# Optimization experiments

Measured on AMD Instinct MI355X. Metric: run time of the kernel, lower is better.

Reference implementation:

```python
import jax, jax.numpy as jnp
import numpy as np

B, T, HID = 2, 4096, 1024
NH, DK, DV = 8, 128, 128
CONV_K = 4
CHUNK = 64


def short_conv_silu(x, w):
    # causal depthwise conv1d, x: [B,T,D], w: [D,K]
    K = w.shape[1]
    xp = jnp.pad(x, ((0, 0), (K - 1, 0), (0, 0)))
    out = sum(xp[:, i:i + x.shape[1], :] * w[:, i] for i in range(K))
    return jax.nn.silu(out)


def hadamard_fm(x, w1, b1, w2, b2):
    # per-head feature map: Linear(x)*Linear(x), x: [B,T,H,D]
    return (jnp.einsum('bthd,ed->bthe', x, w1) + b1) * (jnp.einsum('bthd,ed->bthe', x, w2) + b2)


def chunk_linear_attn(q, k, v, scale):
    # causal linear attention via chunked scan. q,k,v: [B,T,H,D]
    Bq, Tq, H, Dk = q.shape
    Dv = v.shape[-1]
    nc = Tq // CHUNK
    q = (q * scale).reshape(Bq, nc, CHUNK, H, Dk).transpose(1, 0, 2, 3, 4)
    k = k.reshape(Bq, nc, CHUNK, H, Dk).transpose(1, 0, 2, 3, 4)
    v = v.reshape(Bq, nc, CHUNK, H, Dv).transpose(1, 0, 2, 3, 4)
    mask = jnp.tril(jnp.ones((CHUNK, CHUNK), dtype=bool))

    def step(S, inp):
        qc, kc, vc = inp  # [B,C,H,D]
        attn = jnp.einsum('bihk,bjhk->bhij', qc, kc)
        attn = jnp.where(mask, attn, 0.0)
        o = jnp.einsum('bhij,bjhv->bihv', attn, vc) + jnp.einsum('bihk,bhkv->bihv', qc, S)
        S = S + jnp.einsum('bihk,bihv->bhkv', kc, vc)
        return S, o

    S0 = jnp.zeros((Bq, H, Dk, Dv), q.dtype)
    _, o = jax.lax.scan(step, S0, (q, k, v))  # o: [nc,B,C,H,Dv]
    return o.transpose(1, 0, 2, 3, 4).reshape(Bq, Tq, H, Dv)


def setup_inputs() -> dict:
    key = jax.random.key(0)
    ks = jax.random.split(key, 16)
    s = 0.02
    inp = {
        'hidden_states': jax.random.normal(ks[0], (B, T, HID), jnp.float32),
        'wq': jax.random.normal(ks[1], (HID, HID), jnp.float32) * s,
        'wk': jax.random.normal(ks[2], (HID, HID), jnp.float32) * s,
        'wv': jax.random.normal(ks[3], (HID, HID), jnp.float32) * s,
        'wo': jax.random.normal(ks[4], (HID, HID), jnp.float32) * s,
        'conv_q': jax.random.normal(ks[5], (HID, CONV_K), jnp.float32) * 0.2,
        'conv_k': jax.random.normal(ks[6], (HID, CONV_K), jnp.float32) * 0.2,
        'conv_v': jax.random.normal(ks[7], (HID, CONV_K), jnp.float32) * 0.2,
        'fmq_w1': jax.random.normal(ks[8], (DK, DK), jnp.float32) * s,
        'fmq_b1': jnp.zeros((DK,), jnp.float32),
        'fmq_w2': jax.random.normal(ks[9], (DK, DK), jnp.float32) * s,
        'fmq_b2': jnp.zeros((DK,), jnp.float32),
        'fmk_w1': jax.random.normal(ks[10], (DK, DK), jnp.float32) * s,
        'fmk_b1': jnp.zeros((DK,), jnp.float32),
        'fmk_w2': jax.random.normal(ks[11], (DK, DK), jnp.float32) * s,
        'fmk_b2': jnp.zeros((DK,), jnp.float32),
    }
    return inp


def reference(hidden_states, wq, wk, wv, wo, conv_q, conv_k, conv_v,
              fmq_w1, fmq_b1, fmq_w2, fmq_b2, fmk_w1, fmk_b1, fmk_w2, fmk_b2):
    q = short_conv_silu(hidden_states @ wq.T, conv_q)
    k = short_conv_silu(hidden_states @ wk.T, conv_k)
    v = short_conv_silu(hidden_states @ wv.T, conv_v)
    q = q.reshape(B, T, NH, DK)
    k = k.reshape(B, T, NH, DK)
    v = v.reshape(B, T, NH, DV)
    q = hadamard_fm(q, fmq_w1, fmq_b1, fmq_w2, fmq_b2)
    k = hadamard_fm(k, fmk_w1, fmk_b1, fmk_w2, fmk_b2)
    scale = DK ** -0.5
    o = chunk_linear_attn(q, k, v, scale)
    return o.reshape(B, T, NH * DV) @ wo.T
```

## Files before the change

kernel.cpp:

```cpp
#include <hip/hip_runtime.h>
#include <cstdint>
#include <cstddef>

#define T_SEQ 4096
#define BATCH 2
#define HIDDEN 1024
#define NHEAD 8
#define DKV 128
#define BT (BATCH * T_SEQ)
#define NCH 64
#define CHUNK_L 64
#define QSCALE 0.08838834764831845f
#define SCALE_P 1024.0f
#define SCALE_O 8192.0f
#define OEPS 0.7071067811865476f

typedef _Float16 half8 __attribute__((ext_vector_type(8)));
typedef float floatx4 __attribute__((ext_vector_type(4)));

union HBits { _Float16 h; unsigned short u; };

__global__ void cast_f32_f16(const float* __restrict__ X, _Float16* __restrict__ Y, int n8)
{
    int idx = blockIdx.x * 256 + threadIdx.x;
    if (idx < n8) {
        float4 a = ((const float4*)X)[idx * 2];
        float4 b = ((const float4*)X)[idx * 2 + 1];
        half8 h = { (_Float16)a.x, (_Float16)a.y, (_Float16)a.z, (_Float16)a.w,
                    (_Float16)b.x, (_Float16)b.y, (_Float16)b.z, (_Float16)b.w };
        *(half8*)&Y[idx * 8] = h;
    }
}

__global__ void cast8_f32_f16(const float* __restrict__ s0, const float* __restrict__ s1,
                              const float* __restrict__ s2, const float* __restrict__ s3,
                              const float* __restrict__ s4, const float* __restrict__ s5,
                              const float* __restrict__ s6, const float* __restrict__ s7,
                              _Float16* __restrict__ d0, _Float16* __restrict__ d1,
                              _Float16* __restrict__ d2, _Float16* __restrict__ d3,
                              _Float16* __restrict__ d4, _Float16* __restrict__ d5,
                              _Float16* __restrict__ d6, _Float16* __restrict__ d7,
                              int nbig, int nsmall)
{
    int sel = blockIdx.y;
    const float* src; _Float16* dst; int n8;
    switch (sel) {
        case 0: src = s0; dst = d0; n8 = nbig; break;
        case 1: src = s1; dst = d1; n8 = nbig; break;
        case 2: src = s2; dst = d2; n8 = nbig; break;
        case 3: src = s3; dst = d3; n8 = nbig; break;
        case 4: src = s4; dst = d4; n8 = nsmall; break;
        case 5: src = s5; dst = d5; n8 = nsmall; break;
        case 6: src = s6; dst = d6; n8 = nsmall; break;
        default: src = s7; dst = d7; n8 = nsmall; break;
    }
    int idx = blockIdx.x * 256 + threadIdx.x;
    if (idx < n8) {
        float4 u = ((const float4*)src)[idx * 2];
        float4 v = ((const float4*)src)[idx * 2 + 1];
        half8 h = { (_Float16)u.x, (_Float16)u.y, (_Float16)u.z, (_Float16)u.w,
                    (_Float16)v.x, (_Float16)v.y, (_Float16)v.z, (_Float16)v.w };
        *(half8*)&dst[idx * 8] = h;
    }
}

__global__ __launch_bounds__(256) void gemm_nt_f16_h16(const _Float16* __restrict__ A,
                                                       const _Float16* __restrict__ W,
                                                       _Float16* __restrict__ C,
                                                       int M, int N, int K)
{
    __shared__ _Float16 As[128 * 64];
    __shared__ _Float16 Ws[128 * 64];
    const int nwg = gridDim.x * gridDim.y;
    const int bid = blockIdx.y * gridDim.x + blockIdx.x;
    const int swz = (bid & 7) * (nwg >> 3) + (bid >> 3);
    const int bm = (swz / gridDim.x) * 128;
    const int bn = (swz % gridDim.x) * 128;
    const int tid = threadIdx.x;
    const int w = tid >> 6;
    const int l = tid & 63;
    const int wm = (w >> 1) * 64;
    const int wn = (w & 1) * 64;
    const int lane16 = l & 15;
    const int quad = l >> 4;
    const int srow = w * 8 + (l >> 3);
    const int skh = ((l & 7) ^ (l >> 3)) * 8;
    const int rsw = lane16 & 7;

    floatx4 acc[4][4];
#pragma unroll
    for (int i = 0; i < 4; ++i)
#pragma unroll
        for (int j = 0; j < 4; ++j)
            acc[i][j] = (floatx4){0.f, 0.f, 0.f, 0.f};

    for (int k0 = 0; k0 < K; k0 += 64) {
#pragma unroll
        for (int c = 0; c < 4; ++c) {
            int row = c * 32 + srow;
            const _Float16* ga = A + (size_t)(bm + row) * K + k0 + skh;
            const _Float16* gw = W + (size_t)(bn + row) * K + k0 + skh;
            __builtin_amdgcn_global_load_lds(
                (const __attribute__((address_space(1))) void*)ga,
                (__attribute__((address_space(3))) void*)(As + c * 2048 + w * 512), 16, 0, 0);
            __builtin_amdgcn_global_load_lds(
                (const __attribute__((address_space(1))) void*)gw,
                (__attribute__((address_space(3))) void*)(Ws + c * 2048 + w * 512), 16, 0, 0);
        }
        __syncthreads();

#pragma unroll
        for (int s = 0; s < 2; ++s) {
            const int pc = (((s * 4 + quad) ^ rsw)) * 8;
            half8 a[4], b[4];
#pragma unroll
            for (int i = 0; i < 4; ++i) {
                a[i] = *(const half8*)&As[(wm + i * 16 + lane16) * 64 + pc];
                b[i] = *(const half8*)&Ws[(wn + i * 16 + lane16) * 64 + pc];
            }
#pragma unroll
            for (int i = 0; i < 4; ++i)
#pragma unroll
                for (int j = 0; j < 4; ++j)
                    acc[i][j] = __builtin_amdgcn_mfma_f32_16x16x32_f16(a[i], b[j], acc[i][j], 0, 0, 0);
        }
        __syncthreads();
    }
#pragma unroll
    for (int i = 0; i < 4; ++i)
#pragma unroll
        for (int j = 0; j < 4; ++j)
#pragma unroll
            for (int r = 0; r < 4; ++r)
                C[(size_t)(bm + wm + i * 16 + quad * 4 + r) * N + bn + wn + j * 16 + lane16] =
                    (_Float16)acc[i][j][r];
}

__global__ __launch_bounds__(256) void gemm_nt_f16_f32(const _Float16* __restrict__ A,
                                                       const _Float16* __restrict__ W,
                                                       float* __restrict__ C,
                                                       int M, int N, int K, float scale)
{
    __shared__ _Float16 As[128 * 64];
    __shared__ _Float16 Ws[128 * 64];
    const int nwg = gridDim.x * gridDim.y;
    const int bid = blockIdx.y * gridDim.x + blockIdx.x;
    const int swz = (bid & 7) * (nwg >> 3) + (bid >> 3);
    const int bm = (swz / gridDim.x) * 128;
    const int bn = (swz % gridDim.x) * 128;
    const int tid = threadIdx.x;
    const int w = tid >> 6;
    const int l = tid & 63;
    const int wm = (w >> 1) * 64;
    const int wn = (w & 1) * 64;
    const int lane16 = l & 15;
    const int quad = l >> 4;
    const int srow = w * 8 + (l >> 3);
    const int skh = ((l & 7) ^ (l >> 3)) * 8;
    const int rsw = lane16 & 7;

    floatx4 acc[4][4];
#pragma unroll
    for (int i = 0; i < 4; ++i)
#pragma unroll
        for (int j = 0; j < 4; ++j)
            acc[i][j] = (floatx4){0.f, 0.f, 0.f, 0.f};

    for (int k0 = 0; k0 < K; k0 += 64) {
#pragma unroll
        for (int c = 0; c < 4; ++c) {
            int row = c * 32 + srow;
            const _Float16* ga = A + (size_t)(bm + row) * K + k0 + skh;
            const _Float16* gw = W + (size_t)(bn + row) * K + k0 + skh;
            __builtin_amdgcn_global_load_lds(
                (const __attribute__((address_space(1))) void*)ga,
                (__attribute__((address_space(3))) void*)(As + c * 2048 + w * 512), 16, 0, 0);
            __builtin_amdgcn_global_load_lds(
                (const __attribute__((address_space(1))) void*)gw,
                (__attribute__((address_space(3))) void*)(Ws + c * 2048 + w * 512), 16, 0, 0);
        }
        __syncthreads();

#pragma unroll
        for (int s = 0; s < 2; ++s) {
            const int pc = (((s * 4 + quad) ^ rsw)) * 8;
            half8 a[4], b[4];
#pragma unroll
            for (int i = 0; i < 4; ++i) {
                a[i] = *(const half8*)&As[(wm + i * 16 + lane16) * 64 + pc];
                b[i] = *(const half8*)&Ws[(wn + i * 16 + lane16) * 64 + pc];
            }
#pragma unroll
            for (int i = 0; i < 4; ++i)
#pragma unroll
                for (int j = 0; j < 4; ++j)
                    acc[i][j] = __builtin_amdgcn_mfma_f32_16x16x32_f16(a[i], b[j], acc[i][j], 0, 0, 0);
        }
        __syncthreads();
    }
#pragma unroll
    for (int i = 0; i < 4; ++i)
#pragma unroll
        for (int j = 0; j < 4; ++j)
#pragma unroll
            for (int r = 0; r < 4; ++r)
                C[(size_t)(bm + wm + i * 16 + quad * 4 + r) * N + bn + wn + j * 16 + lane16] =
                    acc[i][j][r] * scale;
}

__global__ __launch_bounds__(256) void conv_silu_T(const _Float16* __restrict__ X, int ldx,
                                                   const float* __restrict__ Wc,
                                                   _Float16* __restrict__ VT)
{
    __shared__ _Float16 xs[67 * 64];
    const int bx = blockIdx.x;
    const int t0 = (bx & 63) * 64;
    const int dt = ((bx >> 6) & 15) * 64;
    const int z = bx >> 10;
    const int tid = threadIdx.x;

#pragma unroll
    for (int i = 0; i < 3; ++i) {
        int p = tid + 256 * i;
        if (p < 536) {
            int row = p >> 3, d8 = (p & 7) * 8;
            int t = t0 - 3 + row;
            half8 v;
            if (t >= 0)
                v = *(const half8*)&X[((size_t)z * T_SEQ + t) * ldx + dt + d8];
            else
                v = (half8){0, 0, 0, 0, 0, 0, 0, 0};
            *(half8*)&xs[row * 64 + d8] = v;
        }
    }
    __syncthreads();

    const int d = tid & 63;
    const int dg = dt + d;
    float4 w = *(const float4*)&Wc[dg * 4];
#pragma unroll
    for (int u = 0; u < 2; ++u) {
        int tg = (tid >> 6) + u * 4;
        half8 o;
#pragma unroll
        for (int s = 0; s < 8; ++s) {
            int base = (tg * 8 + s + 3) * 64 + d;
            float acc = (float)xs[base] * w.w
                      + (float)xs[base - 64] * w.z
                      + (float)xs[base - 128] * w.y
                      + (float)xs[base - 192] * w.x;
            o[s] = (_Float16)(acc / (1.f + __expf(-acc)));
        }
        *(half8*)&VT[((size_t)z * HIDDEN + dg) * T_SEQ + t0 + tg * 8] = o;
    }
}

#define XIN_LD 136
__global__ __launch_bounds__(256) void convfm(const _Float16* __restrict__ QKV, int ldx,
                                              const float* __restrict__ Wcq,
                                              const float* __restrict__ Wck,
                                              const _Float16* __restrict__ Wfm,
                                              const float* __restrict__ Bq1,
                                              const float* __restrict__ Bq2,
                                              const float* __restrict__ Bk1,
                                              const float* __restrict__ Bk2,
                                              _Float16* __restrict__ OUTq,
                                              _Float16* __restrict__ OUTk)
{
    const int sel = blockIdx.z;
    const float* Wc = sel ? Wck : Wcq;
    const _Float16* W1h = Wfm + (sel ? 2 * 16384 : 0);
    const _Float16* W2h = Wfm + (sel ? 3 * 16384 : 16384);
    const float* B1 = sel ? Bk1 : Bq1;
    const float* B2 = sel ? Bk2 : Bq2;
    _Float16* OUT = sel ? OUTk : OUTq;

    __shared__ _Float16 xin[67 * XIN_LD];
    __shared__ _Float16 xs[4 * 64 * 32];
    const int t0 = blockIdx.x * 64;
    const int h = blockIdx.y;
    const int tid = threadIdx.x;
    const int w = tid >> 6;
    const int l = tid & 63;
    const int lane16 = l & 15;
    const int quad = l >> 4;
    const bool batch_start = (t0 & (T_SEQ - 1)) == 0;
    const int ebase = w * 32 + lane16;

    half8 pb1[2], pb2[2];
    float b1v[2], b2v[2];
#pragma unroll
    for (int nt = 0; nt < 2; ++nt) {
        pb1[nt] = *(const half8*)&W1h[(size_t)(ebase + nt * 16) * DKV + quad * 8];
        pb2[nt] = *(const half8*)&W2h[(size_t)(ebase + nt * 16) * DKV + quad * 8];
        b1v[nt] = B1[ebase + nt * 16];
        b2v[nt] = B2[ebase + nt * 16];
    }

    for (int p = tid; p < 67 * 16; p += 256) {
        int row = p >> 4, cg = p & 15;
        half8 v;
        if (batch_start && row < 3)
            v = (half8){0, 0, 0, 0, 0, 0, 0, 0};
        else
            v = *(const half8*)&QKV[(size_t)(t0 - 3 + row) * ldx + sel * HIDDEN + h * DKV + cg * 8];
        *(half8*)&xin[row * XIN_LD + cg * 8] = v;
    }
    __syncthreads();

    {
        const int doct = tid & 15;
        const int d0 = doct * 8;
        const int rq = (tid >> 4) * 4;
        const int u = doct >> 2;
        const int col = d0 & 31;

        float w0[8], w1[8], w2[8], w3[8];
#pragma unroll
        for (int e = 0; e < 8; ++e) {
            float4 wv = *(const float4*)&Wc[(h * DKV + d0 + e) * 4];
            w0[e] = wv.x; w1[e] = wv.y; w2[e] = wv.z; w3[e] = wv.w;
        }

#pragma unroll
        for (int rr = 0; rr < 4; ++rr) {
            const int row = rq + rr;
            half8 x3 = *(const half8*)&xin[(row + 0) * XIN_LD + d0];
            half8 x2 = *(const half8*)&xin[(row + 1) * XIN_LD + d0];
            half8 x1 = *(const half8*)&xin[(row + 2) * XIN_LD + d0];
            half8 x0 = *(const half8*)&xin[(row + 3) * XIN_LD + d0];
            half8 o;
#pragma unroll
            for (int e = 0; e < 8; ++e) {
                float acc = fmaf((float)x0[e], w3[e],
                            fmaf((float)x1[e], w2[e],
                            fmaf((float)x2[e], w1[e], (float)x3[e] * w0[e])));
                o[e] = (_Float16)(acc / (1.f + __expf(-acc)));
            }
            *(half8*)&xs[u * 2048 + row * 32 + col] = o;
        }
    }
    __syncthreads();

    floatx4 acc1[4][2], acc2[4][2];
#pragma unroll
    for (int i = 0; i < 4; ++i)
#pragma unroll
        for (int j = 0; j < 2; ++j) {
            acc1[i][j] = (floatx4){0.f, 0.f, 0.f, 0.f};
            acc2[i][j] = (floatx4){0.f, 0.f, 0.f, 0.f};
        }

#pragma unroll
    for (int s = 0; s < 4; ++s) {
        half8 nb1[2], nb2[2];
        if (s < 3) {
#pragma unroll
            for (int nt = 0; nt < 2; ++nt) {
                nb1[nt] = *(const half8*)&W1h[(size_t)(ebase + nt * 16) * DKV + (s + 1) * 32 + quad * 8];
                nb2[nt] = *(const half8*)&W2h[(size_t)(ebase + nt * 16) * DKV + (s + 1) * 32 + quad * 8];
            }
        }
        half8 a[4];
#pragma unroll
        for (int mt = 0; mt < 4; ++mt)
            a[mt] = *(const half8*)&xs[s * 2048 + (mt * 16 + lane16) * 32 + quad * 8];
#pragma unroll
        for (int nt = 0; nt < 2; ++nt) {
#pragma unroll
            for (int mt = 0; mt < 4; ++mt) {
                acc1[mt][nt] = __builtin_amdgcn_mfma_f32_16x16x32_f16(a[mt], pb1[nt], acc1[mt][nt], 0, 0, 0);
                acc2[mt][nt] = __builtin_amdgcn_mfma_f32_16x16x32_f16(a[mt], pb2[nt], acc2[mt][nt], 0, 0, 0);
            }
        }
        if (s < 3) {
            pb1[0] = nb1[0]; pb1[1] = nb1[1];
            pb2[0] = nb2[0]; pb2[1] = nb2[1];
        }
    }

#pragma unroll
    for (int nt = 0; nt < 2; ++nt) {
#pragma unroll
        for (int mt = 0; mt < 4; ++mt)
#pragma unroll
            for (int r = 0; r < 4; ++r) {
                float o = (acc1[mt][nt][r] + b1v[nt]) * (acc2[mt][nt][r] + b2v[nt]);
                OUT[(size_t)(t0 + mt * 16 + quad * 4 + r) * HIDDEN + h * DKV + ebase + nt * 16] = (_Float16)o;
            }
    }
}

__global__ __launch_bounds__(256) void ktv_mfma(const _Float16* __restrict__ Kf,
                                                const _Float16* __restrict__ VT,
                                                _Float16* __restrict__ G16)
{
    __shared__ _Float16 kt[128 * 72];
    const int c = blockIdx.x;
    const int bh = blockIdx.y;
    const int b = bh >> 3, h = bh & 7;
    const int tid = threadIdx.x;
    const int w = tid >> 6;
    const int l = tid & 63;
    const int lane16 = l & 15;
    const int quad = l >> 4;
    const size_t rowbase = (size_t)b * T_SEQ + (size_t)c * CHUNK_L;

    const int m0 = (w >> 1) * 64;
    const int n0 = (w & 1) * 64;
    half8 vta[2][4];
#pragma unroll
    for (int s = 0; s < 2; ++s)
#pragma unroll
        for (int mt = 0; mt < 4; ++mt) {
            int dv = m0 + mt * 16 + lane16;
            vta[s][mt] = *(const half8*)&VT[((size_t)bh * DKV + dv) * T_SEQ + c * CHUNK_L + s * 32 + quad * 8];
        }

    {
        const int dk0 = (tid >> 4) * 8;
        const int jb = (tid & 15) * 4;
        half8 r0 = *(const half8*)&Kf[(rowbase + jb + 0) * HIDDEN + h * DKV + dk0];
        half8 r1 = *(const half8*)&Kf[(rowbase + jb + 1) * HIDDEN + h * DKV + dk0];
        half8 r2 = *(const half8*)&Kf[(rowbase + jb + 2) * HIDDEN + h * DKV + dk0];
        half8 r3 = *(const half8*)&Kf[(rowbase + jb + 3) * HIDDEN + h * DKV + dk0];
#pragma unroll
        for (int dk = 0; dk < 8; ++dk) {
            HBits a0, a1, a2, a3;
            a0.h = r0[dk]; a1.h = r1[dk]; a2.h = r2[dk]; a3.h = r3[dk];
            unsigned int lo = ((unsigned int)a1.u << 16) | a0.u;
            unsigned int hi = ((unsigned int)a3.u << 16) | a2.u;
            *(unsigned int*)&kt[(dk0 + dk) * 72 + jb] = lo;
            *(unsigned int*)&kt[(dk0 + dk) * 72 + jb + 2] = hi;
        }
    }
    __syncthreads();

    floatx4 acc[4][4];
#pragma unroll
    for (int i = 0; i < 4; ++i)
#pragma unroll
        for (int j = 0; j < 4; ++j)
            acc[i][j] = (floatx4){0.f, 0.f, 0.f, 0.f};

#pragma unroll
    for (int s = 0; s < 2; ++s) {
        half8 bb[4];
#pragma unroll
        for (int nt = 0; nt < 4; ++nt)
            bb[nt] = *(const half8*)&kt[(n0 + nt * 16 + lane16) * 72 + s * 32 + quad * 8];
#pragma unroll
        for (int mt = 0; mt < 4; ++mt)
#pragma unroll
            for (int nt = 0; nt < 4; ++nt)
                acc[mt][nt] = __builtin_amdgcn_mfma_f32_16x16x32_f16(vta[s][mt], bb[nt], acc[mt][nt], 0, 0, 0);
    }

    _Float16* Gp = G16 + ((size_t)bh * NCH + c) * (DKV * DKV);
#pragma unroll
    for (int mt = 0; mt < 4; ++mt)
#pragma unroll
        for (int nt = 0; nt < 4; ++nt)
#pragma unroll
            for (int r = 0; r < 4; ++r)
                Gp[(size_t)(m0 + mt * 16 + quad * 4 + r) * DKV + n0 + nt * 16 + lane16] =
                    (_Float16)acc[mt][nt][r];
}

__global__ void prefix_kernel(const _Float16* __restrict__ G16, _Float16* __restrict__ Gh)
{
    int idx = blockIdx.x * 256 + threadIdx.x;
    int bh = idx >> 14;
    int e = idx & 16383;
    const _Float16* p = G16 + (size_t)bh * NCH * 16384 + e;
    _Float16* q = Gh + (size_t)bh * NCH * 16384 + e;
    float run = 0.f;
#pragma unroll
    for (int c = 0; c < NCH; ++c) {
        q[(size_t)c * 16384] = (_Float16)(run * SCALE_P);
        run += (float)p[(size_t)c * 16384];
    }
}

#define PSLD 40
__global__ __launch_bounds__(256) void attn_mfma(const _Float16* __restrict__ Qf,
                                                 const _Float16* __restrict__ Kf,
                                                 const _Float16* __restrict__ VT,
                                                 const _Float16* __restrict__ Gh,
                                                 _Float16* __restrict__ O)
{
    __shared__ _Float16 ps[2 * 64 * PSLD];
    const int c = blockIdx.x;
    const int bh = blockIdx.y;
    const int b = bh >> 3, h = bh & 7;
    const int tid = threadIdx.x;
    const int w = tid >> 6;
    const int l = tid & 63;
    const int lane16 = l & 15;
    const int quad = l >> 4;
    const size_t rowbase = (size_t)b * T_SEQ + (size_t)c * CHUNK_L;
    const int n0o = w * 32;
    const _Float16* gh = Gh + ((size_t)bh * NCH + c) * (DKV * DKV);

    half8 vtpre[2][2];
#pragma unroll
    for (int s = 0; s < 2; ++s)
#pragma unroll
        for (int nt = 0; nt < 2; ++nt) {
            int dv = n0o + nt * 16 + lane16;
            vtpre[s][nt] = *(const half8*)&VT[((size_t)bh * DKV + dv) * T_SEQ + c * CHUNK_L + s * 32 + quad * 8];
        }
    half8 ghp[2];
#pragma unroll
    for (int nt = 0; nt < 2; ++nt)
        ghp[nt] = *(const half8*)&gh[(size_t)(n0o + nt * 16 + lane16) * DKV + quad * 8];

    {
        const int m0 = (w >> 1) * 32;
        const int n0 = (w & 1) * 32;
        floatx4 aq[2][2];
#pragma unroll
        for (int i = 0; i < 2; ++i)
#pragma unroll
            for (int j = 0; j < 2; ++j)
                aq[i][j] = (floatx4){0.f, 0.f, 0.f, 0.f};
#pragma unroll
        for (int s = 0; s < 4; ++s) {
            half8 a[2], bb[2];
#pragma unroll
            for (int mt = 0; mt < 2; ++mt)
                a[mt] = *(const half8*)&Qf[(rowbase + m0 + mt * 16 + lane16) * HIDDEN +
                                           h * DKV + s * 32 + quad * 8];
#pragma unroll
            for (int nt = 0; nt < 2; ++nt)
                bb[nt] = *(const half8*)&Kf[(rowbase + n0 + nt * 16 + lane16) * HIDDEN +
                                            h * DKV + s * 32 + quad * 8];
#pragma unroll
            for (int mt = 0; mt < 2; ++mt)
#pragma unroll
                for (int nt = 0; nt < 2; ++nt)
                    aq[mt][nt] = __builtin_amdgcn_mfma_f32_16x16x32_f16(a[mt], bb[nt], aq[mt][nt], 0, 0, 0);
        }
#pragma unroll
        for (int mt = 0; mt < 2; ++mt)
#pragma unroll
            for (int nt = 0; nt < 2; ++nt) {
                int j = n0 + nt * 16 + lane16;
#pragma unroll
                for (int r = 0; r < 4; ++r) {
                    int i = m0 + mt * 16 + quad * 4 + r;
                    float v = (j <= i) ? aq[mt][nt][r] * SCALE_P : 0.f;
                    ps[(j >> 5) * 64 * PSLD + i * PSLD + (j & 31)] = (_Float16)v;
                }
            }
    }
    __syncthreads();

    floatx4 accO[4][2];
#pragma unroll
    for (int i = 0; i < 4; ++i)
#pragma unroll
        for (int j = 0; j < 2; ++j)
            accO[i][j] = (floatx4){0.f, 0.f, 0.f, 0.f};

#pragma unroll
    for (int s = 0; s < 2; ++s) {
        half8 a[4];
#pragma unroll
        for (int mt = 0; mt < 4; ++mt)
            a[mt] = *(const half8*)&ps[s * 64 * PSLD + (mt * 16 + lane16) * PSLD + quad * 8];
#pragma unroll
        for (int mt = 0; mt < 4; ++mt)
#pragma unroll
            for (int nt = 0; nt < 2; ++nt)
                accO[mt][nt] = __builtin_amdgcn_mfma_f32_16x16x32_f16(a[mt], vtpre[s][nt], accO[mt][nt], 0, 0, 0);
    }

#pragma unroll
    for (int s = 0; s < 4; ++s) {
        half8 nb[2];
        if (s < 3) {
#pragma unroll
            for (int nt = 0; nt < 2; ++nt)
                nb[nt] = *(const half8*)&gh[(size_t)(n0o + nt * 16 + lane16) * DKV + (s + 1) * 32 + quad * 8];
        }
        half8 a[4];
#pragma unroll
        for (int mt = 0; mt < 4; ++mt)
            a[mt] = *(const half8*)&Qf[(rowbase + mt * 16 + lane16) * HIDDEN +
                                       h * DKV + s * 32 + quad * 8];
#pragma unroll
        for (int mt = 0; mt < 4; ++mt)
#pragma unroll
            for (int nt = 0; nt < 2; ++nt)
                accO[mt][nt] = __builtin_amdgcn_mfma_f32_16x16x32_f16(a[mt], ghp[nt], accO[mt][nt], 0, 0, 0);
        if (s < 3) { ghp[0] = nb[0]; ghp[1] = nb[1]; }
    }

#pragma unroll
    for (int mt = 0; mt < 4; ++mt)
#pragma unroll
        for (int nt = 0; nt < 2; ++nt)
#pragma unroll
            for (int r = 0; r < 4; ++r)
                O[(rowbase + mt * 16 + quad * 4 + r) * HIDDEN + h * DKV + n0o + nt * 16 + lane16] =
                    (_Float16)(accO[mt][nt][r] * OEPS);
}

extern "C" void kernel_launch(void* const* d_in, const int* in_sizes, int n_in,
                              void* d_out, int out_size, void* d_ws, size_t ws_size,
                              hipStream_t stream)
{
    (void)in_sizes; (void)n_in; (void)out_size; (void)ws_size;
    const float* hs = (const float*)d_in[0];
    const float* wq = (const float*)d_in[1];
    const float* wk = (const float*)d_in[2];
    const float* wv = (const float*)d_in[3];
    const float* wo = (const float*)d_in[4];
    const float* cq = (const float*)d_in[5];
    const float* ck = (const float*)d_in[6];
    const float* cv = (const float*)d_in[7];
    const float* fmq_w1 = (const float*)d_in[8];
    const float* fmq_b1 = (const float*)d_in[9];
    const float* fmq_w2 = (const float*)d_in[10];
    const float* fmq_b2 = (const float*)d_in[11];
    const float* fmk_w1 = (const float*)d_in[12];
    const float* fmk_b1 = (const float*)d_in[13];
    const float* fmk_w2 = (const float*)d_in[14];
    const float* fmk_b2 = (const float*)d_in[15];
    float* out = (float*)d_out;
    char* ws = (char*)d_ws;

    const size_t MB = 1024 * 1024;
    _Float16* h16     = (_Float16*)(ws + 0);
    _Float16* qf16    = (_Float16*)(ws + 0);
    _Float16* wqkv16  = (_Float16*)(ws + 16 * MB);
    _Float16* wo16    = wqkv16 + (3 << 20);
    _Float16* fmw     = wqkv16 + (4 << 20);
    _Float16* qkvlin  = (_Float16*)(ws + 32 * MB);
    _Float16* kf16    = (_Float16*)(ws + 80 * MB);
    _Float16* vT      = (_Float16*)(ws + 96 * MB);
    _Float16* O16     = (_Float16*)(ws + 112 * MB);
    _Float16* G16     = (_Float16*)(ws + 128 * MB);
    _Float16* Gh      = (_Float16*)(ws + 160 * MB);

    cast_f32_f16<<<4096, 256, 0, stream>>>(hs, h16, BT * HIDDEN / 8);
    cast8_f32_f16<<<dim3(512, 8), 256, 0, stream>>>(
        wq, wk, wv, wo, fmq_w1, fmq_w2, fmk_w1, fmk_w2,
        wqkv16, wqkv16 + (1 << 20), wqkv16 + (2 << 20), wo16,
        fmw, fmw + 16384, fmw + 2 * 16384, fmw + 3 * 16384,
        HIDDEN * HIDDEN / 8, DKV * DKV / 8);

    dim3 gqkv(3 * HIDDEN / 128, BT / 128);
    gemm_nt_f16_h16<<<gqkv, 256, 0, stream>>>(h16, wqkv16, qkvlin, BT, 3 * HIDDEN, HIDDEN);

    conv_silu_T<<<2048, 256, 0, stream>>>(qkvlin + 2 * HIDDEN, 3 * HIDDEN, cv, vT);

    dim3 fg(BT / 64, NHEAD, 2);
    convfm<<<fg, 256, 0, stream>>>(qkvlin, 3 * HIDDEN, cq, ck, fmw,
                                   fmq_b1, fmq_b2, fmk_b1, fmk_b2, qf16, kf16);

    dim3 ag(NCH, BATCH * NHEAD);
    ktv_mfma<<<ag, 256, 0, stream>>>(kf16, vT, G16);
    prefix_kernel<<<(16 * 16384) / 256, 256, 0, stream>>>(G16, Gh);
    attn_mfma<<<ag, 256, 0, stream>>>(qf16, kf16, vT, Gh, O16);

    dim3 gg(HIDDEN / 128, BT / 128);
    gemm_nt_f16_f32<<<gg, 256, 0, stream>>>(O16, wo16, out, BT, HIDDEN, HIDDEN, 1.0f / SCALE_O);
}
```

Baseline: 313.4 us.

## Pipeline QKV GEMM with 256x128 double-buffered tiles and vectorize prefix scan

Replaces the QKV projection GEMM with a 512-thread 256x128 tile kernel. It double-buffers A and W tiles in LDS and interleaves async global-to-LDS loads with MFMA phases, using explicit waitcnt, barriers and setprio. The goal is to hide load latency and raise data reuse, at the cost of more LDS and register pressure and fragile manual synchronisation. It also removes the block-index swizzle from the output GEMM and vectorizes the chunk prefix-sum kernel so each thread handles four elements.

```diff
diff --git a/kernel.cpp b/kernel.cpp
--- a/kernel.cpp
+++ b/kernel.cpp
@@ -16,6 +16,7 @@
 #define OEPS 0.7071067811865476f
 
 typedef _Float16 half8 __attribute__((ext_vector_type(8)));
+typedef _Float16 half4 __attribute__((ext_vector_type(4)));
 typedef float floatx4 __attribute__((ext_vector_type(4)));
 
 union HBits { _Float16 h; unsigned short u; };
@@ -64,28 +65,35 @@
     }
 }
 
-__global__ __launch_bounds__(256) void gemm_nt_f16_h16(const _Float16* __restrict__ A,
-                                                       const _Float16* __restrict__ W,
-                                                       _Float16* __restrict__ C,
-                                                       int M, int N, int K)
-{
-    __shared__ _Float16 As[128 * 64];
-    __shared__ _Float16 Ws[128 * 64];
-    const int nwg = gridDim.x * gridDim.y;
-    const int bid = blockIdx.y * gridDim.x + blockIdx.x;
-    const int swz = (bid & 7) * (nwg >> 3) + (bid >> 3);
-    const int bm = (swz / gridDim.x) * 128;
-    const int bn = (swz % gridDim.x) * 128;
+#define A_TILE_H (256 * 64)
+#define W_TILE_H (128 * 64)
+
+__global__ __launch_bounds__(512, 2) void gemm256x128_nt_f16_h16(
+    const _Float16* __restrict__ A, const _Float16* __restrict__ W,
+    _Float16* __restrict__ C, int M, int N, int K)
+{
+    __shared__ _Float16 As[2 * A_TILE_H];
+    __shared__ _Float16 Ws[2 * W_TILE_H];
+    const int bm = blockIdx.y * 256;
+    const int bn = blockIdx.x * 128;
     const int tid = threadIdx.x;
     const int w = tid >> 6;
     const int l = tid & 63;
+    const int lane16 = l & 15;
+    const int quad = l >> 4;
     const int wm = (w >> 1) * 64;
     const int wn = (w & 1) * 64;
-    const int lane16 = l & 15;
-    const int quad = l >> 4;
-    const int srow = w * 8 + (l >> 3);
-    const int skh = ((l & 7) ^ (l >> 3)) * 8;
-    const int rsw = lane16 & 7;
+    const int NT = K >> 6;
+
+    const int srow8 = tid >> 3;
+    const int sch = (tid & 7) ^ (srow8 & 7);
+
+#define STG(src, baseRow, k0, q, dstBase)                                            \
+    __builtin_amdgcn_global_load_lds(                                                \
+        (const __attribute__((address_space(1))) void*)((src) +                      \
+            (size_t)((baseRow) + (q) * 64 + srow8) * K + (k0) + sch * 8),            \
+        (__attribute__((address_space(3))) void*)((dstBase) + (q) * 4096 + w * 512), \
+        16, 0, 0)
 
     floatx4 acc[4][4];
 #pragma unroll
@@ -94,46 +102,97 @@
         for (int j = 0; j < 4; ++j)
             acc[i][j] = (floatx4){0.f, 0.f, 0.f, 0.f};
 
-    for (int k0 = 0; k0 < K; k0 += 64) {
-#pragma unroll
-        for (int c = 0; c < 4; ++c) {
-            int row = c * 32 + srow;
-            const _Float16* ga = A + (size_t)(bm + row) * K + k0 + skh;
-            const _Float16* gw = W + (size_t)(bn + row) * K + k0 + skh;
-            __builtin_amdgcn_global_load_lds(
-                (const __attribute__((address_space(1))) void*)ga,
-                (__attribute__((address_space(3))) void*)(As + c * 2048 + w * 512), 16, 0, 0);
-            __builtin_amdgcn_global_load_lds(
-                (const __attribute__((address_space(1))) void*)gw,
-                (__attribute__((address_space(3))) void*)(Ws + c * 2048 + w * 512), 16, 0, 0);
-        }
-        __syncthreads();
-
-#pragma unroll
-        for (int s = 0; s < 2; ++s) {
-            const int pc = (((s * 4 + quad) ^ rsw)) * 8;
-            half8 a[4], b[4];
-#pragma unroll
-            for (int i = 0; i < 4; ++i) {
-                a[i] = *(const half8*)&As[(wm + i * 16 + lane16) * 64 + pc];
-                b[i] = *(const half8*)&Ws[(wn + i * 16 + lane16) * 64 + pc];
-            }
-#pragma unroll
-            for (int i = 0; i < 4; ++i)
-#pragma unroll
-                for (int j = 0; j < 4; ++j)
-                    acc[i][j] = __builtin_amdgcn_mfma_f32_16x16x32_f16(a[i], b[j], acc[i][j], 0, 0, 0);
-        }
-        __syncthreads();
-    }
-#pragma unroll
-    for (int i = 0; i < 4; ++i)
-#pragma unroll
-        for (int j = 0; j < 4; ++j)
+    {
+        STG(W, bn, 0, 0, Ws); STG(W, bn, 0, 1, Ws);
+#pragma unroll
+        for (int q = 0; q < 4; ++q) STG(A, bm, 0, q, As);
+        if (NT > 1) {
+            STG(W, bn, 64, 0, Ws + W_TILE_H); STG(W, bn, 64, 1, Ws + W_TILE_H);
+            asm volatile("s_waitcnt vmcnt(2)" ::: "memory");
+        } else {
+            asm volatile("s_waitcnt vmcnt(0)" ::: "memory");
+        }
+        __builtin_amdgcn_s_barrier();
+        asm volatile("" ::: "memory");
+    }
+
+    for (int t = 0; t < NT; ++t) {
+        const int bs = t & 1;
+        const _Float16* Asb = As + bs * A_TILE_H;
+        const _Float16* Wsb = Ws + bs * W_TILE_H;
+        _Float16* AsN = As + (bs ^ 1) * A_TILE_H;
+        _Float16* WsN = Ws + bs * W_TILE_H;
+        const int kA = (t + 1) << 6;
+        const int kW = (t + 2) << 6;
+        const bool doA = (t + 1) < NT;
+        const bool doW = (t + 2) < NT;
+
+        half8 a[4][2], b[4][2];
+
+#pragma unroll
+        for (int mt = 0; mt < 4; ++mt)
+#pragma unroll
+            for (int ks = 0; ks < 2; ++ks) {
+                int row = wm + mt * 16 + lane16;
+                a[mt][ks] = *(const half8*)&Asb[row * 64 + (((ks * 4 + quad) ^ (row & 7)) << 3)];
+            }
+#pragma unroll
+        for (int nt = 0; nt < 2; ++nt)
+#pragma unroll
+            for (int ks = 0; ks < 2; ++ks) {
+                int row = wn + nt * 16 + lane16;
+                b[nt][ks] = *(const half8*)&Wsb[row * 64 + (((ks * 4 + quad) ^ (row & 7)) << 3)];
+            }
+        if (doA) { STG(A, bm, kA, 0, AsN); STG(A, bm, kA, 1, AsN); }
+        asm volatile("s_waitcnt lgkmcnt(8)" ::: "memory");
+        __builtin_amdgcn_s_barrier();
+        asm volatile("s_waitcnt lgkmcnt(0)" ::: "memory");
+        __builtin_amdgcn_s_setprio(1);
+#pragma unroll
+        for (int ks = 0; ks < 2; ++ks)
+#pragma unroll
+            for (int mt = 0; mt < 4; ++mt)
+#pragma unroll
+                for (int nt = 0; nt < 2; ++nt)
+                    acc[mt][nt] = __builtin_amdgcn_mfma_f32_16x16x32_f16(a[mt][ks], b[nt][ks], acc[mt][nt], 0, 0, 0);
+        __builtin_amdgcn_s_setprio(0);
+        __builtin_amdgcn_s_barrier();
+
+#pragma unroll
+        for (int nt = 2; nt < 4; ++nt)
+#pragma unroll
+            for (int ks = 0; ks < 2; ++ks) {
+                int row = wn + nt * 16 + lane16;
+                b[nt][ks] = *(const half8*)&Wsb[row * 64 + (((ks * 4 + quad) ^ (row & 7)) << 3)];
+            }
+        if (doA) { STG(A, bm, kA, 2, AsN); STG(A, bm, kA, 3, AsN); }
+        __builtin_amdgcn_s_barrier();
+        asm volatile("s_waitcnt lgkmcnt(0)" ::: "memory");
+        __builtin_amdgcn_s_setprio(1);
+#pragma unroll
+        for (int ks = 0; ks < 2; ++ks)
+#pragma unroll
+            for (int mt = 0; mt < 4; ++mt)
+#pragma unroll
+                for (int nt = 2; nt < 4; ++nt)
+                    acc[mt][nt] = __builtin_amdgcn_mfma_f32_16x16x32_f16(a[mt][ks], b[nt][ks], acc[mt][nt], 0, 0, 0);
+        __builtin_amdgcn_s_setprio(0);
+        if (doW) { STG(W, bn, kW, 0, WsN); STG(W, bn, kW, 1, WsN); }
+        if (doW)      asm volatile("s_waitcnt vmcnt(2)" ::: "memory");
+        else if (doA) asm volatile("s_waitcnt vmcnt(0)" ::: "memory");
+        __builtin_amdgcn_s_barrier();
+        asm volatile("" ::: "memory");
+    }
+#undef STG
+
+#pragma unroll
+    for (int mt = 0; mt < 4; ++mt)
+#pragma unroll
+        for (int nt = 0; nt < 4; ++nt)
 #pragma unroll
             for (int r = 0; r < 4; ++r)
-                C[(size_t)(bm + wm + i * 16 + quad * 4 + r) * N + bn + wn + j * 16 + lane16] =
-                    (_Float16)acc[i][j][r];
+                C[(size_t)(bm + wm + mt * 16 + quad * 4 + r) * N + bn + wn + nt * 16 + lane16] =
+                    (_Float16)acc[mt][nt][r];
 }
 
 __global__ __launch_bounds__(256) void gemm_nt_f16_f32(const _Float16* __restrict__ A,
@@ -143,11 +202,8 @@
 {
     __shared__ _Float16 As[128 * 64];
     __shared__ _Float16 Ws[128 * 64];
-    const int nwg = gridDim.x * gridDim.y;
-    const int bid = blockIdx.y * gridDim.x + blockIdx.x;
-    const int swz = (bid & 7) * (nwg >> 3) + (bid >> 3);
-    const int bm = (swz / gridDim.x) * 128;
-    const int bn = (swz % gridDim.x) * 128;
+    const int bm = blockIdx.y * 128;
+    const int bn = blockIdx.x * 128;
     const int tid = threadIdx.x;
     const int w = tid >> 6;
     const int l = tid & 63;
@@ -470,15 +526,18 @@
 __global__ void prefix_kernel(const _Float16* __restrict__ G16, _Float16* __restrict__ Gh)
 {
     int idx = blockIdx.x * 256 + threadIdx.x;
-    int bh = idx >> 14;
-    int e = idx & 16383;
-    const _Float16* p = G16 + (size_t)bh * NCH * 16384 + e;
-    _Float16* q = Gh + (size_t)bh * NCH * 16384 + e;
-    float run = 0.f;
-#pragma unroll
+    int bh = idx >> 12;
+    int e4 = (idx & 4095) * 4;
+    const _Float16* p = G16 + (size_t)bh * NCH * 16384 + e4;
+    _Float16* q = Gh + (size_t)bh * NCH * 16384 + e4;
+    float r0 = 0.f, r1 = 0.f, r2 = 0.f, r3 = 0.f;
+#pragma unroll 8
     for (int c = 0; c < NCH; ++c) {
-        q[(size_t)c * 16384] = (_Float16)(run * SCALE_P);
-        run += (float)p[(size_t)c * 16384];
+        half4 g = *(const half4*)&p[(size_t)c * 16384];
+        half4 o = { (_Float16)(r0 * SCALE_P), (_Float16)(r1 * SCALE_P),
+                    (_Float16)(r2 * SCALE_P), (_Float16)(r3 * SCALE_P) };
+        *(half4*)&q[(size_t)c * 16384] = o;
+        r0 += (float)g[0]; r1 += (float)g[1]; r2 += (float)g[2]; r3 += (float)g[3];
     }
 }
 
@@ -651,8 +710,8 @@
         fmw, fmw + 16384, fmw + 2 * 16384, fmw + 3 * 16384,
         HIDDEN * HIDDEN / 8, DKV * DKV / 8);
 
-    dim3 gqkv(3 * HIDDEN / 128, BT / 128);
-    gemm_nt_f16_h16<<<gqkv, 256, 0, stream>>>(h16, wqkv16, qkvlin, BT, 3 * HIDDEN, HIDDEN);
+    dim3 gqkv(3 * HIDDEN / 128, BT / 256);
+    gemm256x128_nt_f16_h16<<<gqkv, 512, 0, stream>>>(h16, wqkv16, qkvlin, BT, 3 * HIDDEN, HIDDEN);
 
     conv_silu_T<<<2048, 256, 0, stream>>>(qkvlin + 2 * HIDDEN, 3 * HIDDEN, cv, vT);
 
@@ -662,7 +721,7 @@
 
     dim3 ag(NCH, BATCH * NHEAD);
     ktv_mfma<<<ag, 256, 0, stream>>>(kf16, vT, G16);
-    prefix_kernel<<<(16 * 16384) / 256, 256, 0, stream>>>(G16, Gh);
+    prefix_kernel<<<256, 256, 0, stream>>>(G16, Gh);
     attn_mfma<<<ag, 256, 0, stream>>>(qf16, kf16, vT, Gh, O16);
 
     dim3 gg(HIDDEN / 128, BT / 128);
```

New measurement: 320.8 us. 2.4% more time.
